# Optimization experiments

Hardware: AMD Instinct MI355X
Metric: run time of the kernel (lower is better)

Reference implementation:

```python
import jax, jax.numpy as jnp
import numpy as np

E = 262144   # number of edges
B = 8192     # buckets per grouping
D = 32       # uniform bucket degree (B*D == E)
DIM = 128    # in_feats
OUT = 128    # out_feats


def setup_inputs() -> dict:
    key = jax.random.key(0)
    ks = jax.random.split(key, 12)
    src_feat = jax.random.normal(ks[0], (E, DIM), jnp.float32)
    dst_feat = jax.random.normal(ks[1], (E, DIM), jnp.float32)
    timestamp = jax.random.uniform(ks[2], (E,), jnp.float32) * 100.0
    # grouping permutations: flat edge order -> buckets of uniform degree
    src_perm = jax.random.permutation(ks[3], E).astype(jnp.int32)
    dst_perm = jax.random.permutation(ks[4], E).astype(jnp.int32)
    # causal deg_indices: index of most recent valid temporal neighbor, <= position
    pos = jnp.arange(D, dtype=jnp.int32)[None, :]
    src_deg_indices = jnp.minimum(jax.random.randint(ks[5], (B, D), 0, D, jnp.int32), pos)
    dst_deg_indices = jnp.minimum(jax.random.randint(ks[6], (B, D), 0, D, jnp.int32), pos)
    # TimeEncodingLayer('cosine') params
    basis_freq = 0.1 * jnp.linspace(0.0, 9.0, DIM, dtype=jnp.float32)
    phase = jnp.zeros((DIM,), jnp.float32)
    W_time = jax.random.normal(ks[7], (DIM, 2 * DIM), jnp.float32) * 0.05
    b_time = jnp.zeros((DIM,), jnp.float32)
    # fc_self / fc_neigh
    W_self = jax.random.normal(ks[8], (OUT, DIM), jnp.float32) * 0.05
    b_self = jnp.zeros((OUT,), jnp.float32)
    W_neigh = jax.random.normal(ks[9], (OUT, DIM), jnp.float32) * 0.05
    b_neigh = jnp.zeros((OUT,), jnp.float32)
    return dict(src_feat=src_feat, dst_feat=dst_feat, timestamp=timestamp,
                basis_freq=basis_freq, phase=phase, W_time=W_time, b_time=b_time,
                W_self=W_self, b_self=b_self, W_neigh=W_neigh, b_neigh=b_neigh,
                src_perm=src_perm, dst_perm=dst_perm,
                src_deg_indices=src_deg_indices, dst_deg_indices=dst_deg_indices)


def _encode_time(u, t, basis_freq, phase, W_time, b_time):
    # cosine time encoding: cos(t * freq + phase), concat with u, linear, relu
    tt = jnp.cos(t[:, None] * basis_freq[None, :] + phase[None, :])  # [E, DIM]
    x = jnp.concatenate([u, tt], axis=-1) @ W_time.T + b_time
    return jax.nn.relu(x)


def _mean_conv(h_self_e, h_neigh_e, perm, idx, W_self, b_self, W_neigh, b_neigh):
    # gather flat edge features into [B, D, DIM] buckets
    hs = h_self_e[perm].reshape(B, D, DIM)
    hn = h_neigh_e[perm].reshape(B, D, DIM)
    # mean aggregator: cumsum / (deg_indices+1), then gather at deg_indices
    mean_cof = (idx.astype(hn.dtype) + 1.0)[:, :, None]          # [B, D, 1]
    h_feat = jnp.cumsum(hn, axis=1) / mean_cof                    # [B, D, DIM]
    mask_feat = jnp.take_along_axis(h_feat, idx[:, :, None], axis=1)  # [B, D, DIM]
    rst = hs @ W_self.T + b_self + mask_feat @ W_neigh.T + b_neigh    # [B, D, OUT]
    # scatter back to flat edge order
    return jnp.zeros((E, OUT), rst.dtype).at[perm].set(rst.reshape(E, OUT))


def reference(src_feat, dst_feat, timestamp, basis_freq, phase, W_time, b_time,
              W_self, b_self, W_neigh, b_neigh,
              src_perm, dst_perm, src_deg_indices, dst_deg_indices):
    enc_src = _encode_time(src_feat, timestamp, basis_freq, phase, W_time, b_time)
    enc_dst = _encode_time(dst_feat, timestamp, basis_freq, phase, W_time, b_time)
    # groupby='src': self = src embedding, neighbors = dst embeddings
    src_out = _mean_conv(enc_src, enc_dst, src_perm, src_deg_indices,
                         W_self, b_self, W_neigh, b_neigh)
    # groupby='dst': self = dst embedding, neighbors = src embeddings
    dst_out = _mean_conv(enc_dst, enc_src, dst_perm, dst_deg_indices,
                         W_self, b_self, W_neigh, b_neigh)
    return src_out, dst_out
```

## Files before the change

kernel.cpp:

```cpp
#include <hip/hip_runtime.h>
#include <hip/hip_bf16.h>
#include <math.h>

#define E_EDGES 262144
#define NBUCKET 8192
#define DEG     32
#define FDIM    128

typedef float f32x4 __attribute__((ext_vector_type(4)));
typedef short s16x8 __attribute__((ext_vector_type(8)));
typedef short s16x4 __attribute__((ext_vector_type(4)));

typedef const __attribute__((address_space(1))) unsigned g_u32;
typedef __attribute__((address_space(3))) unsigned l_u32;

__device__ __forceinline__ short f2bf(float f) {
    __hip_bfloat16 h = __float2bfloat16(f);
    return *reinterpret_cast<short*>(&h);
}
__device__ __forceinline__ float bf2f(short s) {
    union { unsigned u; float f; } v; v.u = ((unsigned)(unsigned short)s) << 16;
    return v.f;
}

__device__ __forceinline__ s16x8 read_wfrag(const short* w_lds, int n, int k0) {
    int byte = ((n << 8) + (k0 << 1)) ^ ((n & 7) << 4);
    return *reinterpret_cast<const s16x8*>(reinterpret_cast<const char*>(w_lds) + byte);
}

__device__ __forceinline__ void stage_w(short* w_lds, const float* __restrict__ Wg,
                                        int stride, int tid) {
    #pragma unroll
    for (int it = 0; it < 16; ++it) {
        int i  = it * 256 + tid;
        int n  = i >> 5;
        int k4 = (i & 31) << 2;
        const float4 v = *reinterpret_cast<const float4*>(Wg + (size_t)n * stride + k4);
        s16x4 h; h[0]=f2bf(v.x); h[1]=f2bf(v.y); h[2]=f2bf(v.z); h[3]=f2bf(v.w);
        int byte = ((n << 8) + (k4 << 1)) ^ ((n & 7) << 4);
        *reinterpret_cast<s16x4*>(reinterpret_cast<char*>(w_lds) + byte) = h;
    }
}

__device__ __forceinline__ void dma_w32k(const short* __restrict__ gsw, short* lds, int tid) {
    const int lane = tid & 63, wid = tid >> 6;
    const char* g = reinterpret_cast<const char*>(gsw);
    char* l = reinterpret_cast<char*>(lds);
    #pragma unroll
    for (int i = 0; i < 8; ++i) {
        const int off = i * 4096 + wid * 1024;
        __builtin_amdgcn_global_load_lds((g_u32*)(g + off + lane * 16),
                                         (l_u32*)(l + off), 16, 0, 0);
    }
}

__global__ void prep_kernel(const float* __restrict__ W_time,
                            const float* __restrict__ W_self,
                            const float* __restrict__ W_neigh,
                            short* __restrict__ Wswz)
{
    const int t = blockIdx.x * 256 + threadIdx.x;
    const int region = t >> 11;
    const int chunk  = t & 2047;
    const int n = chunk >> 4;
    const int c = chunk & 15;

    const float* src;
    if      (region == 0) src = W_time  + n * 256 + c * 8;
    else if (region == 1) src = W_time  + n * 256 + 128 + c * 8;
    else if (region == 2) src = W_self  + n * 128 + c * 8;
    else                  src = W_neigh + n * 128 + c * 8;

    const float4 lo = *reinterpret_cast<const float4*>(src);
    const float4 hi = *reinterpret_cast<const float4*>(src + 4);
    s16x8 h;
    h[0]=f2bf(lo.x); h[1]=f2bf(lo.y); h[2]=f2bf(lo.z); h[3]=f2bf(lo.w);
    h[4]=f2bf(hi.x); h[5]=f2bf(hi.y); h[6]=f2bf(hi.z); h[7]=f2bf(hi.w);

    const int byte = (region << 15) + ((((n << 8) + (c << 4)) ^ ((n & 7) << 4)));
    *reinterpret_cast<s16x8*>(reinterpret_cast<char*>(Wswz) + byte) = h;
}

__global__ __launch_bounds__(512, 2)
void encode_kernel(const float* __restrict__ src_feat,
                   const float* __restrict__ dst_feat,
                   const float* __restrict__ ts,
                   const float* __restrict__ freq,
                   const float* __restrict__ ph,
                   const short* __restrict__ Wswz,
                   const float* __restrict__ b_time,
                   short* __restrict__ enc_src,
                   short* __restrict__ enc_dst)
{
    __shared__ short w_lds[2][128 * 128];

    const int tid  = threadIdx.x;
    const int lane = tid & 63;
    const int wid  = tid >> 6;
    const int lrow = lane & 15;
    const int q    = lane >> 4;
    const int klo  = q << 3;
    const int r0   = blockIdx.x * 128 + wid * 16;

    float4 sf[8], df[8];
    #pragma unroll
    for (int kb = 0; kb < 4; ++kb) {
        const float* ps = src_feat + (size_t)(r0 + lrow) * FDIM + kb * 32 + klo;
        const float* pd = dst_feat + (size_t)(r0 + lrow) * FDIM + kb * 32 + klo;
        sf[kb*2]   = *reinterpret_cast<const float4*>(ps);
        sf[kb*2+1] = *reinterpret_cast<const float4*>(ps + 4);
        df[kb*2]   = *reinterpret_cast<const float4*>(pd);
        df[kb*2+1] = *reinterpret_cast<const float4*>(pd + 4);
    }

    {
        const char* g = reinterpret_cast<const char*>(Wswz);
        char* l = reinterpret_cast<char*>(&w_lds[0][0]);
        #pragma unroll
        for (int i = 0; i < 8; ++i) {
            const int off = i * 8192 + wid * 1024;
            __builtin_amdgcn_global_load_lds((g_u32*)(g + off + lane * 16),
                                             (l_u32*)(l + off), 16, 0, 0);
        }
    }

    const float t_row = ts[r0 + lrow];
    s16x8 tf[4];
    #pragma unroll
    for (int kb = 0; kb < 4; ++kb) {
        s16x8 t;
        #pragma unroll
        for (int j = 0; j < 8; ++j) {
            const int k = kb * 32 + klo + j;
            t[j] = f2bf(__cosf(fmaf(t_row, freq[k], ph[k])));
        }
        tf[kb] = t;
    }

    s16x8 as_[4], ad_[4];
    #pragma unroll
    for (int kb = 0; kb < 4; ++kb) {
        s16x8 a, b;
        #pragma unroll
        for (int j = 0; j < 4; ++j) {
            a[j]   = f2bf(sf[kb*2][j]);   a[4+j] = f2bf(sf[kb*2+1][j]);
            b[j]   = f2bf(df[kb*2][j]);   b[4+j] = f2bf(df[kb*2+1][j]);
        }
        as_[kb] = a; ad_[kb] = b;
    }
    __syncthreads();

    #pragma unroll
    for (int nt = 0; nt < 8; ++nt) {
        const int n = nt * 16 + lrow;
        f32x4 a = {0.f, 0.f, 0.f, 0.f};
        #pragma unroll
        for (int kb = 0; kb < 4; ++kb)
            a = __builtin_amdgcn_mfma_f32_16x16x32_bf16(
                    read_wfrag(w_lds[1], n, kb * 32 + klo), tf[kb], a, 0, 0, 0);
        f32x4 b = a;
        #pragma unroll
        for (int kb = 0; kb < 4; ++kb) {
            const s16x8 wf = read_wfrag(w_lds[0], n, kb * 32 + klo);
            a = __builtin_amdgcn_mfma_f32_16x16x32_bf16(wf, as_[kb], a, 0, 0, 0);
            b = __builtin_amdgcn_mfma_f32_16x16x32_bf16(wf, ad_[kb], b, 0, 0, 0);
        }
        const int ch = nt * 16 + q * 4;
        const float4 bias4 = *reinterpret_cast<const float4*>(b_time + ch);
        s16x4 ss, sd;
        #pragma unroll
        for (int r = 0; r < 4; ++r) {
            float es = a[r] + bias4[r]; es = es > 0.f ? es : 0.f;
            float ed = b[r] + bias4[r]; ed = ed > 0.f ? ed : 0.f;
            ss[r] = f2bf(es); sd[r] = f2bf(ed);
        }
        *reinterpret_cast<s16x4*>(enc_src + (size_t)(r0 + lrow) * FDIM + ch) = ss;
        *reinterpret_cast<s16x4*>(enc_dst + (size_t)(r0 + lrow) * FDIM + ch) = sd;
    }
}

__global__ __launch_bounds__(256, 2)
void encode_fallback(const float* __restrict__ src_feat,
                     const float* __restrict__ dst_feat,
                     const float* __restrict__ ts,
                     const float* __restrict__ freq,
                     const float* __restrict__ ph,
                     const float* __restrict__ W_time,
                     const float* __restrict__ b_time,
                     short* __restrict__ enc_src,
                     short* __restrict__ enc_dst)
{
    __shared__ short w_lds[128 * 128];
    const int tid  = threadIdx.x;
    const int lane = tid & 63;
    const int wid  = tid >> 6;
    const int r0   = blockIdx.x * 64 + wid * 16;
    const int lrow = lane & 15;
    const int klo  = (lane >> 4) << 3;

    stage_w(w_lds, W_time + 128, 256, tid);
    const float t_row = ts[r0 + lrow];
    s16x8 tf[4];
    #pragma unroll
    for (int kb = 0; kb < 4; ++kb) {
        const int k = kb * 32 + klo;
        s16x8 t;
        #pragma unroll
        for (int j = 0; j < 8; ++j)
            t[j] = f2bf(__cosf(fmaf(t_row, freq[k + j], ph[k + j])));
        tf[kb] = t;
    }
    __syncthreads();
    f32x4 S[8];
    #pragma unroll
    for (int nt = 0; nt < 8; ++nt) {
        f32x4 a = {0.f, 0.f, 0.f, 0.f};
        #pragma unroll
        for (int kb = 0; kb < 4; ++kb)
            a = __builtin_amdgcn_mfma_f32_16x16x32_bf16(
                    tf[kb], read_wfrag(w_lds, nt * 16 + lrow, kb * 32 + klo), a, 0, 0, 0);
        S[nt] = a;
    }
    __syncthreads();
    stage_w(w_lds, W_time, 256, tid);
    __syncthreads();
    #pragma unroll
    for (int s = 0; s < 2; ++s) {
        const float* feat = s ? dst_feat : src_feat;
        short*       enc  = s ? enc_dst  : enc_src;
        s16x8 af[4];
        #pragma unroll
        for (int kb = 0; kb < 4; ++kb) {
            const float* p = feat + (size_t)(r0 + lrow) * FDIM + kb * 32 + klo;
            const float4 lo = *reinterpret_cast<const float4*>(p);
            const float4 hi = *reinterpret_cast<const float4*>(p + 4);
            s16x8 a;
            a[0]=f2bf(lo.x); a[1]=f2bf(lo.y); a[2]=f2bf(lo.z); a[3]=f2bf(lo.w);
            a[4]=f2bf(hi.x); a[5]=f2bf(hi.y); a[6]=f2bf(hi.z); a[7]=f2bf(hi.w);
            af[kb] = a;
        }
        #pragma unroll
        for (int nt = 0; nt < 8; ++nt) {
            f32x4 acc = S[nt];
            #pragma unroll
            for (int kb = 0; kb < 4; ++kb)
                acc = __builtin_amdgcn_mfma_f32_16x16x32_bf16(
                        af[kb], read_wfrag(w_lds, nt * 16 + lrow, kb * 32 + klo), acc, 0, 0, 0);
            const int col  = nt * 16 + lrow;
            const float bias = b_time[col];
            const int rbase = r0 + ((lane >> 4) << 2);
            #pragma unroll
            for (int r = 0; r < 4; ++r) {
                float e = acc[r] + bias;
                e = e > 0.f ? e : 0.f;
                enc[(size_t)(rbase + r) * FDIM + col] = f2bf(e);
            }
        }
    }
}

template<int DMA>
__global__ __launch_bounds__(256, 3)
void conv_kernel(const short* __restrict__ enc_src,
                 const short* __restrict__ enc_dst,
                 const short* __restrict__ Wswz_self,
                 const short* __restrict__ Wswz_neigh,
                 const float* __restrict__ W_self,
                 const float* __restrict__ W_neigh,
                 const float* __restrict__ b_self,
                 const float* __restrict__ b_neigh,
                 const int* __restrict__ src_perm,
                 const int* __restrict__ dst_perm,
                 const int* __restrict__ src_idx,
                 const int* __restrict__ dst_idx,
                 float* __restrict__ out)
{
    __shared__ short w_lds[128 * 128];
    __shared__ short hf[2][DEG * 128];
    __shared__ int   perm_s[2][DEG];
    __shared__ int   idx_s[2][DEG];
    __shared__ float bias_s[128];

    const int tid = threadIdx.x;
    const int g   = blockIdx.y;
    const int b0  = blockIdx.x * 2;

    const short* enc_self  = g ? enc_dst : enc_src;
    const short* enc_neigh = g ? enc_src : enc_dst;
    const int*   perm      = g ? dst_perm : src_perm;
    const int*   degi      = g ? dst_idx  : src_idx;
    float*       outg      = out + (size_t)g * E_EDGES * FDIM;

    if (DMA) dma_w32k(Wswz_self, w_lds, tid);

    if (tid < 64) {
        const int lb = tid >> 5, d = tid & 31;
        perm_s[lb][d] = perm[(b0 + lb) * DEG + d];
        idx_s[lb][d]  = degi[(b0 + lb) * DEG + d];
    } else if (tid < 192) {
        const int c = tid - 64;
        bias_s[c] = b_self[c] + b_neigh[c];
    }
    if (!DMA) stage_w(w_lds, W_self, 128, tid);
    __syncthreads();

    const int lane = tid & 63;
    const int wid  = tid >> 6;
    const int lb   = wid >> 1;
    const int mt   = wid & 1;
    const int lrow = lane & 15;
    const int klo  = (lane >> 4) << 3;
    const int row  = mt * 16 + lrow;

    s16x8 hsf[4];
    {
        const int e = perm_s[lb][row];
        const short* p = enc_self + (size_t)e * FDIM;
        #pragma unroll
        for (int kb = 0; kb < 4; ++kb)
            hsf[kb] = *reinterpret_cast<const s16x8*>(p + kb * 32 + klo);
    }

    const int lbc = tid >> 7;
    const int c   = tid & 127;
    unsigned short cum[DEG];
    #pragma unroll
    for (int d = 0; d < DEG; ++d) {
        const int e = perm_s[lbc][d];
        cum[d] = *reinterpret_cast<const unsigned short*>(
                     enc_neigh + (size_t)e * FDIM + c);
    }

    f32x4 acc[8];
    #pragma unroll
    for (int nt = 0; nt < 8; ++nt) {
        f32x4 a = {0.f, 0.f, 0.f, 0.f};
        #pragma unroll
        for (int kb = 0; kb < 4; ++kb)
            a = __builtin_amdgcn_mfma_f32_16x16x32_bf16(
                    hsf[kb], read_wfrag(w_lds, nt * 16 + lrow, kb * 32 + klo), a, 0, 0, 0);
        acc[nt] = a;
    }

    {
        float run = 0.f;
        #pragma unroll
        for (int d = 0; d < DEG; ++d) {
            run += bf2f((short)cum[d]);
            const float inv = __builtin_amdgcn_rcpf((float)(idx_s[lbc][d] + 1));
            const int byte = ((d << 8) + (c << 1)) ^ ((d & 7) << 4);
            *reinterpret_cast<short*>(reinterpret_cast<char*>(hf[lbc]) + byte)
                = f2bf(run * inv);
        }
    }

    __syncthreads();
    if (DMA) dma_w32k(Wswz_neigh, w_lds, tid);
    else     stage_w(w_lds, W_neigh, 128, tid);
    __syncthreads();

    s16x8 mff[4];
    {
        const int j = idx_s[lb][row];
        #pragma unroll
        for (int kb = 0; kb < 4; ++kb) {
            const int byte = ((j << 8) + ((kb * 32 + klo) << 1)) ^ ((j & 7) << 4);
            mff[kb] = *reinterpret_cast<const s16x8*>(
                          reinterpret_cast<const char*>(hf[lb]) + byte);
        }
    }
    #pragma unroll
    for (int nt = 0; nt < 8; ++nt) {
        f32x4 a = acc[nt];
        #pragma unroll
        for (int kb = 0; kb < 4; ++kb)
            a = __builtin_amdgcn_mfma_f32_16x16x32_bf16(
                    mff[kb], read_wfrag(w_lds, nt * 16 + lrow, kb * 32 + klo), a, 0, 0, 0);
        acc[nt] = a;
    }

    __syncthreads();
    {
        float* epl = reinterpret_cast<float*>(w_lds) + wid * 2048;
        #pragma unroll
        for (int nt = 0; nt < 8; ++nt) {
            const int col = nt * 16 + lrow;
            const float bias = bias_s[col];
            #pragma unroll
            for (int r = 0; r < 4; ++r) {
                const int rtile = ((lane >> 4) << 2) + r;
                epl[rtile * 128 + col] = acc[nt][r] + bias;
            }
        }
        asm volatile("s_waitcnt lgkmcnt(0)" ::: "memory");
        __builtin_amdgcn_sched_barrier(0);
        #pragma unroll
        for (int i = 0; i < 8; ++i) {
            const int rtile = i * 2 + (lane >> 5);
            const int c4    = (lane & 31) * 4;
            const f32x4 v = *reinterpret_cast<const f32x4*>(epl + rtile * 128 + c4);
            const int e = perm_s[lb][mt * 16 + rtile];
            *reinterpret_cast<f32x4*>(outg + (size_t)e * FDIM + c4) = v;
        }
    }
}

extern "C" void kernel_launch(void* const* d_in, const int* in_sizes, int n_in,
                              void* d_out, int out_size, void* d_ws, size_t ws_size,
                              hipStream_t stream) {
    (void)in_sizes; (void)n_in; (void)out_size;

    const float* src_feat = (const float*)d_in[0];
    const float* dst_feat = (const float*)d_in[1];
    const float* ts       = (const float*)d_in[2];
    const float* freq     = (const float*)d_in[3];
    const float* ph       = (const float*)d_in[4];
    const float* W_time   = (const float*)d_in[5];
    const float* b_time   = (const float*)d_in[6];
    const float* W_self   = (const float*)d_in[7];
    const float* b_self   = (const float*)d_in[8];
    const float* W_neigh  = (const float*)d_in[9];
    const float* b_neigh  = (const float*)d_in[10];
    const int*   src_perm = (const int*)d_in[11];
    const int*   dst_perm = (const int*)d_in[12];
    const int*   src_idx  = (const int*)d_in[13];
    const int*   dst_idx  = (const int*)d_in[14];

    short* enc_src = (short*)d_ws;
    short* enc_dst = enc_src + (size_t)E_EDGES * FDIM;
    short* Wswz    = enc_dst + (size_t)E_EDGES * FDIM;
    const size_t need = (size_t)E_EDGES * FDIM * 2 * 2 + 4 * 32768;

    if (ws_size >= need) {
        prep_kernel<<<dim3(32), dim3(256), 0, stream>>>(W_time, W_self, W_neigh, Wswz);
        encode_kernel<<<dim3(E_EDGES / 128), dim3(512), 0, stream>>>(
            src_feat, dst_feat, ts, freq, ph, Wswz, b_time, enc_src, enc_dst);
        conv_kernel<1><<<dim3(NBUCKET / 2, 2), dim3(256), 0, stream>>>(
            enc_src, enc_dst, Wswz + 2 * 16384, Wswz + 3 * 16384, W_self, W_neigh,
            b_self, b_neigh, src_perm, dst_perm, src_idx, dst_idx, (float*)d_out);
    } else {
        encode_fallback<<<dim3(E_EDGES / 64), dim3(256), 0, stream>>>(
            src_feat, dst_feat, ts, freq, ph, W_time, b_time, enc_src, enc_dst);
        conv_kernel<0><<<dim3(NBUCKET / 2, 2), dim3(256), 0, stream>>>(
            enc_src, enc_dst, (const short*)nullptr, (const short*)nullptr,
            W_self, W_neigh, b_self, b_neigh,
            src_perm, dst_perm, src_idx, dst_idx, (float*)d_out);
    }
}
```

Before: 239.4 us.

## Halve encode kernel LDS and stage weight loads to raise occupancy

The encode kernel now keeps a single 32KB weight buffer in LDS instead of two. It first computes the time-encoding partial sums with the time half of W_time, then reloads the feature half into the same buffer. The src and dst feature loads are split and staggered to reduce register pressure, and launch bounds go from 2 to 3 blocks per CU. The cost is extra barriers and a serialized second weight DMA, plus partial sums held in registers across phases.

```diff
diff --git a/kernel.cpp b/kernel.cpp
--- a/kernel.cpp
+++ b/kernel.cpp
@@ -49,6 +49,18 @@
     #pragma unroll
     for (int i = 0; i < 8; ++i) {
         const int off = i * 4096 + wid * 1024;
+        __builtin_amdgcn_global_load_lds((g_u32*)(g + off + lane * 16),
+                                         (l_u32*)(l + off), 16, 0, 0);
+    }
+}
+
+__device__ __forceinline__ void dma_w32k_512(const short* __restrict__ gsw, short* lds, int tid) {
+    const int lane = tid & 63, wid = tid >> 6;
+    const char* g = reinterpret_cast<const char*>(gsw);
+    char* l = reinterpret_cast<char*>(lds);
+    #pragma unroll
+    for (int i = 0; i < 4; ++i) {
+        const int off = i * 8192 + wid * 1024;
         __builtin_amdgcn_global_load_lds((g_u32*)(g + off + lane * 16),
                                          (l_u32*)(l + off), 16, 0, 0);
     }
@@ -81,7 +93,7 @@
     *reinterpret_cast<s16x8*>(reinterpret_cast<char*>(Wswz) + byte) = h;
 }
 
-__global__ __launch_bounds__(512, 2)
+__global__ __launch_bounds__(512, 3)
 void encode_kernel(const float* __restrict__ src_feat,
                    const float* __restrict__ dst_feat,
                    const float* __restrict__ ts,
@@ -92,7 +104,7 @@
                    short* __restrict__ enc_src,
                    short* __restrict__ enc_dst)
 {
-    __shared__ short w_lds[2][128 * 128];
+    __shared__ short w_lds[128 * 128];
 
     const int tid  = threadIdx.x;
     const int lane = tid & 63;
@@ -101,30 +113,11 @@
     const int q    = lane >> 4;
     const int klo  = q << 3;
     const int r0   = blockIdx.x * 128 + wid * 16;
-
-    float4 sf[8], df[8];
-    #pragma unroll
-    for (int kb = 0; kb < 4; ++kb) {
-        const float* ps = src_feat + (size_t)(r0 + lrow) * FDIM + kb * 32 + klo;
-        const float* pd = dst_feat + (size_t)(r0 + lrow) * FDIM + kb * 32 + klo;
-        sf[kb*2]   = *reinterpret_cast<const float4*>(ps);
-        sf[kb*2+1] = *reinterpret_cast<const float4*>(ps + 4);
-        df[kb*2]   = *reinterpret_cast<const float4*>(pd);
-        df[kb*2+1] = *reinterpret_cast<const float4*>(pd + 4);
-    }
-
-    {
-        const char* g = reinterpret_cast<const char*>(Wswz);
-        char* l = reinterpret_cast<char*>(&w_lds[0][0]);
-        #pragma unroll
-        for (int i = 0; i < 8; ++i) {
-            const int off = i * 8192 + wid * 1024;
-            __builtin_amdgcn_global_load_lds((g_u32*)(g + off + lane * 16),
-                                             (l_u32*)(l + off), 16, 0, 0);
-        }
-    }
-
-    const float t_row = ts[r0 + lrow];
+    const int row  = r0 + lrow;
+
+    dma_w32k_512(Wswz + 16384, w_lds, tid);
+
+    const float t_row = ts[row];
     s16x8 tf[4];
     #pragma unroll
     for (int kb = 0; kb < 4; ++kb) {
@@ -136,20 +129,9 @@
         }
         tf[kb] = t;
     }
-
-    s16x8 as_[4], ad_[4];
-    #pragma unroll
-    for (int kb = 0; kb < 4; ++kb) {
-        s16x8 a, b;
-        #pragma unroll
-        for (int j = 0; j < 4; ++j) {
-            a[j]   = f2bf(sf[kb*2][j]);   a[4+j] = f2bf(sf[kb*2+1][j]);
-            b[j]   = f2bf(df[kb*2][j]);   b[4+j] = f2bf(df[kb*2+1][j]);
-        }
-        as_[kb] = a; ad_[kb] = b;
-    }
-    __syncthreads();
-
+    __syncthreads();
+
+    f32x4 S[8];
     #pragma unroll
     for (int nt = 0; nt < 8; ++nt) {
         const int n = nt * 16 + lrow;
@@ -157,25 +139,87 @@
         #pragma unroll
         for (int kb = 0; kb < 4; ++kb)
             a = __builtin_amdgcn_mfma_f32_16x16x32_bf16(
-                    read_wfrag(w_lds[1], n, kb * 32 + klo), tf[kb], a, 0, 0, 0);
-        f32x4 b = a;
+                    read_wfrag(w_lds, n, kb * 32 + klo), tf[kb], a, 0, 0, 0);
+        S[nt] = a;
+    }
+    __syncthreads();
+
+    dma_w32k_512(Wswz, w_lds, tid);
+    float4 sf[8];
+    {
+        const float* ps = src_feat + (size_t)row * FDIM + klo;
         #pragma unroll
         for (int kb = 0; kb < 4; ++kb) {
-            const s16x8 wf = read_wfrag(w_lds[0], n, kb * 32 + klo);
-            a = __builtin_amdgcn_mfma_f32_16x16x32_bf16(wf, as_[kb], a, 0, 0, 0);
-            b = __builtin_amdgcn_mfma_f32_16x16x32_bf16(wf, ad_[kb], b, 0, 0, 0);
-        }
+            sf[kb*2]   = *reinterpret_cast<const float4*>(ps + kb * 32);
+            sf[kb*2+1] = *reinterpret_cast<const float4*>(ps + kb * 32 + 4);
+        }
+    }
+    __syncthreads();
+
+    s16x8 af[4];
+    #pragma unroll
+    for (int kb = 0; kb < 4; ++kb) {
+        s16x8 a;
+        #pragma unroll
+        for (int j = 0; j < 4; ++j) {
+            a[j] = f2bf(sf[kb*2][j]); a[4+j] = f2bf(sf[kb*2+1][j]);
+        }
+        af[kb] = a;
+    }
+    float4 df[8];
+    {
+        const float* pd = dst_feat + (size_t)row * FDIM + klo;
+        #pragma unroll
+        for (int kb = 0; kb < 4; ++kb) {
+            df[kb*2]   = *reinterpret_cast<const float4*>(pd + kb * 32);
+            df[kb*2+1] = *reinterpret_cast<const float4*>(pd + kb * 32 + 4);
+        }
+    }
+    #pragma unroll
+    for (int nt = 0; nt < 8; ++nt) {
+        const int n = nt * 16 + lrow;
+        f32x4 a = S[nt];
+        #pragma unroll
+        for (int kb = 0; kb < 4; ++kb)
+            a = __builtin_amdgcn_mfma_f32_16x16x32_bf16(
+                    read_wfrag(w_lds, n, kb * 32 + klo), af[kb], a, 0, 0, 0);
         const int ch = nt * 16 + q * 4;
         const float4 bias4 = *reinterpret_cast<const float4*>(b_time + ch);
-        s16x4 ss, sd;
+        s16x4 ss;
         #pragma unroll
         for (int r = 0; r < 4; ++r) {
-            float es = a[r] + bias4[r]; es = es > 0.f ? es : 0.f;
-            float ed = b[r] + bias4[r]; ed = ed > 0.f ? ed : 0.f;
-            ss[r] = f2bf(es); sd[r] = f2bf(ed);
-        }
-        *reinterpret_cast<s16x4*>(enc_src + (size_t)(r0 + lrow) * FDIM + ch) = ss;
-        *reinterpret_cast<s16x4*>(enc_dst + (size_t)(r0 + lrow) * FDIM + ch) = sd;
+            float e = a[r] + bias4[r]; e = e > 0.f ? e : 0.f;
+            ss[r] = f2bf(e);
+        }
+        *reinterpret_cast<s16x4*>(enc_src + (size_t)row * FDIM + ch) = ss;
+    }
+
+    #pragma unroll
+    for (int kb = 0; kb < 4; ++kb) {
+        s16x8 a;
+        #pragma unroll
+        for (int j = 0; j < 4; ++j) {
+            a[j] = f2bf(df[kb*2][j]); a[4+j] = f2bf(df[kb*2+1][j]);
+        }
+        af[kb] = a;
+    }
+    #pragma unroll
+    for (int nt = 0; nt < 8; ++nt) {
+        const int n = nt * 16 + lrow;
+        f32x4 b = S[nt];
+        #pragma unroll
+        for (int kb = 0; kb < 4; ++kb)
+            b = __builtin_amdgcn_mfma_f32_16x16x32_bf16(
+                    read_wfrag(w_lds, n, kb * 32 + klo), af[kb], b, 0, 0, 0);
+        const int ch = nt * 16 + q * 4;
+        const float4 bias4 = *reinterpret_cast<const float4*>(b_time + ch);
+        s16x4 sd;
+        #pragma unroll
+        for (int r = 0; r < 4; ++r) {
+            float e = b[r] + bias4[r]; e = e > 0.f ? e : 0.f;
+            sd[r] = f2bf(e);
+        }
+        *reinterpret_cast<s16x4*>(enc_dst + (size_t)row * FDIM + ch) = sd;
     }
 }
 
```

After: 264.5 us. 1.1x slower.
